# Kernel optimization log

Measured on AMD Instinct MI355X. Metric: run time of the kernel, lower is better.

## Reference

```python
import jax, jax.numpy as jnp
import numpy as np

J = 24          # SMPL_NR_JOINTS
H = 24          # hidden_dim
D_IN = 3        # input_dim (xyz)
SMPL_PARENTS = [-1, 0, 0, 0, 1, 2, 3, 4, 5, 6, 7, 8, 9, 9, 9, 12, 13, 14, 16, 17, 18, 19, 20, 21]

def _build_A():
    # undirected kinematic tree + self loops, row-normalized (mean aggregation)
    M = np.zeros((J, J), np.float32)
    for child, parent in enumerate(SMPL_PARENTS):
        if parent >= 0:
            M[child, parent] = 1.0
            M[parent, child] = 1.0
    M += np.eye(J, dtype=np.float32)
    M /= M.sum(axis=1, keepdims=True)
    return jnp.asarray(M)

A_NORM = _build_A()  # [J, J]

def setup_inputs() -> dict:
    key = jax.random.key(0)
    ks = jax.random.split(key, 12)
    B, S, T = 2048, 24, 24
    g = lambda k, shape, s=0.1: jax.random.normal(k, shape, dtype=jnp.float32) * s
    return {
        "src": g(ks[0], (B, S, J, D_IN), 1.0),
        "tgt": g(ks[1], (B, T, J, D_IN), 1.0),
        "We": g(ks[2], (H, D_IN)), "be": jnp.zeros((H,), jnp.float32),
        # gate order: 0=i, 1=f, 2=c, 3=o
        "Wxl": g(ks[3], (4, H, H)), "bxl": jnp.zeros((4, H), jnp.float32),
        "Wxr": g(ks[4], (4, H, H)),
        "Whl": g(ks[5], (4, H, H)), "bhl": jnp.zeros((4, H), jnp.float32),
        "Whr": g(ks[6], (4, H, H)),
        "wg": g(ks[7], (3, H)),   # peephole weights for i, f, o
        "bg": jnp.zeros((4, H), jnp.float32),
        "Wd": g(ks[8], (D_IN * J, H * J)), "bd": jnp.zeros((D_IN * J,), jnp.float32),
    }

def _gconv(x, Wl, bl, Wr):
    # x: [B, J, D]; mean-aggregate over fixed 24-node graph, then l(agg) + r(x)
    agg = jnp.einsum('ij,bjd->bid', A_NORM, x)
    return agg @ Wl.T + bl + x @ Wr.T

def _cell(X, h, c, Wxl, bxl, Wxr, Whl, bhl, Whr, wg, bg):
    gx = lambda g: _gconv(X, Wxl[g], bxl[g], Wxr[g])
    gh = lambda g: _gconv(h, Whl[g], bhl[g], Whr[g])
    i = jax.nn.sigmoid(gx(0) + gh(0) + wg[0] * c + bg[0])
    f = jax.nn.sigmoid(gx(1) + gh(1) + wg[1] * c + bg[1])
    c_new = f * c + i * jnp.tanh(gx(2) + gh(2) + bg[2])
    o = jax.nn.sigmoid(gx(3) + gh(3) + wg[2] * c_new + bg[3])
    h_new = o * jnp.tanh(c_new)
    return o, h_new, c_new

def reference(src, tgt, We, be, Wxl, bxl, Wxr, Whl, bhl, Whr, wg, bg, Wd, bd):
    B, S = src.shape[0], src.shape[1]
    T = tgt.shape[1]
    params = (Wxl, bxl, Wxr, Whl, bhl, Whr, wg, bg)
    enc = lambda x: jax.nn.relu(x @ We.T + be)  # [B, J, H]

    # --- warm-up over last 24 src frames (deterministic: encode only first step) ---
    X0 = enc(src[:, S - 24])
    h = jnp.zeros((B, J, H), src.dtype)
    c = jnp.zeros((B, J, H), src.dtype)
    out, h, c = _cell(X0, h, c, *params)

    def warm_step(carry, _):
        o_, h_, c_ = carry
        o_, h_, c_ = _cell(o_, h_, c_, *params)
        return (o_, h_, c_), None
    (out, h, c), _ = jax.lax.scan(warm_step, (out, h, c), None, length=23)

    # --- decode T steps: first input is enc(tgt[:,0]), then feed previous out ---
    out0, h, c = _cell(enc(tgt[:, 0]), h, c, *params)

    def dec_step(carry, _):
        o_, h_, c_ = carry
        o2, h2, c2 = _cell(o_, h_, c_, *params)
        return (o2, h2, c2), o2
    _, rest = jax.lax.scan(dec_step, (out0, h, c), None, length=T - 1)  # [T-1, B, J, H]

    seq = jnp.concatenate([out0[None], rest], axis=0)            # [T, B, J, H]
    outs = seq.transpose(1, 0, 2, 3).reshape(B, T, J * H)        # [B, T, 576]
    return outs @ Wd.T + bd                                      # [B, T, 72]
```

## Files before the change

kernel.cpp:

```cpp
#include <hip/hip_runtime.h>


typedef short  s16x8 __attribute__((ext_vector_type(8)));
typedef float  f32x4 __attribute__((ext_vector_type(4)));
typedef _Float16 f16x8 __attribute__((ext_vector_type(8)));

#define TPB 192
#define NB 2
#define PQ_OFF 0
#define UO_OFF 19968
#define SMEM_SZ 26880

#define BAR() do { asm volatile("s_waitcnt lgkmcnt(0)" ::: "memory"); \
                   __builtin_amdgcn_s_barrier(); } while (0)

#define L2E  1.4426950408889634f
#define L2E2 2.8853900817779268f

__device__ __forceinline__ unsigned short f2h(float f) {
    _Float16 h = (_Float16)f;
    return *(unsigned short*)&h;
}
__device__ __forceinline__ unsigned int pkrtz(float a, float b) {
    auto h = __builtin_amdgcn_cvt_pkrtz(a, b);
    return *(unsigned int*)&h;
}
__device__ __forceinline__ float frcp(float x) { return __builtin_amdgcn_rcpf(x); }

#if __has_builtin(__builtin_amdgcn_exp2f)
#define EXP2(x) __builtin_amdgcn_exp2f(x)
#else
#define EXP2(x) __expf((x) * 0.6931471805599453f)
#endif

__device__ __forceinline__ float sigm2(float y) {
    float t = EXP2(-y);
    return frcp(1.0f + t);
}
__device__ __forceinline__ float tanh2s(float ys) {
    float t = EXP2(fminf(-ys, 86.64f));
    return (1.f - t) * frcp(1.f + t);
}
__device__ __forceinline__ float tanhc(float x) {
    float t = EXP2(fminf(x * -L2E2, 86.64f));
    return (1.f - t) * frcp(1.f + t);
}

#if __has_builtin(__builtin_amdgcn_mov_dpp)
__device__ __forceinline__ float xor8(float v) {
    int r = __builtin_amdgcn_mov_dpp(__float_as_int(v), 0x128, 0xf, 0xf, false);
    return __int_as_float(r);
}
#else
__device__ __forceinline__ float xor8(float v) { return __shfl_xor(v, 8); }
#endif

extern "C" __global__ void __launch_bounds__(TPB, 3)
gclstm_main(const float* __restrict__ src,
            const float* __restrict__ tgt,
            const float* __restrict__ We,
            const float* __restrict__ be,
            const float* __restrict__ Wxl,
            const float* __restrict__ bxl,
            const float* __restrict__ Wxr,
            const float* __restrict__ Whl,
            const float* __restrict__ bhl,
            const float* __restrict__ Whr,
            const float* __restrict__ wg,
            const float* __restrict__ bg,
            unsigned short* __restrict__ seqh)
{
    __shared__ __align__(16) char smem[SMEM_SZ];
    unsigned short* PQt  = (unsigned short*)(smem + PQ_OFF);
    unsigned short* UO   = (unsigned short*)(smem + UO_OFF);
    unsigned int*   UO32 = (unsigned int*)(smem + UO_OFF);

    const int tid = threadIdx.x;
    const int b0 = blockIdx.x * NB;
    const int lane = tid & 63, wid = tid >> 6;
    const int l15 = lane & 15, quad = lane >> 4;

    const int par[24] = {-1,0,0,0,1,2,3,4,5,6,7,8,9,9,9,12,13,14,16,17,18,19,20,21};

    f16x8 w1f[4][2];
#pragma unroll
    for (int cj = 0; cj < 4; ++cj) {
        int np = (wid * 4 + cj) * 16 + l15;
        int path = np >= 96 ? 1 : 0;
        int nn = np - path * 96;
        int g = nn / 24, d = nn - g * 24;
        const float* Wx = path ? Wxr : Wxl;
        const float* Wh = path ? Whr : Whl;
#pragma unroll
        for (int kt = 0; kt < 2; ++kt) {
            f16x8 f;
#pragma unroll
            for (int kk = 0; kk < 8; ++kk) {
                int k = kt * 32 + quad * 8 + kk;
                float v = 0.f;
                if (k < 48) {
                    int df = k >> 1;
                    v = (k & 1) ? Wh[g * 576 + d * 24 + df] : Wx[g * 576 + d * 24 + df];
                }
                f[kk] = (_Float16)v;
            }
            w1f[cj][kt] = f;
        }
    }

    f16x8 mf[3];
    {
        int i = wid * 16 + l15;
        int si = i / 24, ji = i - si * 24;
        int cnt = 1 + (par[ji] >= 0 ? 1 : 0);
#pragma unroll
        for (int ch = 0; ch < 24; ++ch) cnt += (par[ch] == ji) ? 1 : 0;
        float cntf = (float)cnt;
#pragma unroll
        for (int kt = 0; kt < 3; ++kt) {
            f16x8 f;
#pragma unroll
            for (int kk = 0; kk < 8; ++kk) {
                int jp = kt * 32 + quad * 8 + kk;
                int sj = jp / 48;
                int rem = jp - sj * 48;
                int pz = rem / 24;
                int j = rem - pz * 24;
                float v = 0.f;
                if (sj == si) {
                    if (pz == 0) v = (j == ji || par[j] == ji || par[ji] == j) ? 1.f : 0.f;
                    else         v = (j == ji) ? cntf : 0.f;
                }
                f[kk] = (_Float16)v;
            }
            mf[kt] = f;
        }
    }

    const int d1 = l15;
    const int d2 = 16 + (l15 & 7);
    const bool lo = l15 < 8;
    float bC1[4], bC2[4], wv1[3], wv2[3];
#pragma unroll
    for (int g = 0; g < 4; ++g) {
        float sc = (g == 2) ? L2E2 : L2E;
        bC1[g] = (bxl[g * 24 + d1] + bhl[g * 24 + d1] + bg[g * 24 + d1]) * sc;
        bC2[g] = (bxl[g * 24 + d2] + bhl[g * 24 + d2] + bg[g * 24 + d2]) * sc;
    }
#pragma unroll
    for (int p = 0; p < 3; ++p) {
        wv1[p] = wg[p * 24 + d1] * L2E;
        wv2[p] = wg[p * 24 + d2] * L2E;
    }

    int rowR[4];
    float iwR1[4], iwR2[4];
    unsigned int sb[4];
#pragma unroll
    for (int rr = 0; rr < 4; ++rr) {
        int row = wid * 16 + quad * 4 + rr;
        rowR[rr] = row;
        int j = row % 24;
        int cnt = 1 + (par[j] >= 0 ? 1 : 0);
#pragma unroll
        for (int ch = 0; ch < 24; ++ch) cnt += (par[ch] == j) ? 1 : 0;
        float iw = cnt == 2 ? 0.5f : cnt == 3 ? (1.f / 3.f) : cnt == 4 ? 0.25f : 0.2f;
        iwR1[rr] = iw * L2E;
        iwR2[rr] = iw * L2E2;
        sb[rr] = (unsigned int)((b0 + row / 24) * 13824 + j * 24);
    }
    int row2v[2]; float iw2v1[2], iw2v2[2]; unsigned int sb2v[2];
#pragma unroll
    for (int e = 0; e < 2; ++e) {
        int rsel = lo ? e : e + 2;
        row2v[e] = rowR[rsel];
        iw2v1[e] = iwR1[rsel]; iw2v2[e] = iwR2[rsel];
        sb2v[e] = sb[rsel];
    }

    float c1[4] = {0.f, 0.f, 0.f, 0.f};
    float c2[2] = {0.f, 0.f};

#pragma unroll
    for (int t = 0; t < 3; ++t) {
        int task = tid + t * TPB;
        int row = task / 12, dp = task - row * 12;
        int b = b0 + row / 24, j = row % 24;
        const float* sp = src + (size_t)b * 1728 + j * 3;
        float s0 = sp[0], s1 = sp[1], s2 = sp[2];
        int d = 2 * dp;
        float x0 = be[d] + s0 * We[d * 3] + s1 * We[d * 3 + 1] + s2 * We[d * 3 + 2];
        float x1 = be[d + 1] + s0 * We[d * 3 + 3] + s1 * We[d * 3 + 4] + s2 * We[d * 3 + 5];
        x0 = fmaxf(x0, 0.f); x1 = fmaxf(x1, 0.f);
        uint2 wv; wv.x = pkrtz(x0, 0.f); wv.y = pkrtz(x1, 0.f);
        *(uint2*)(UO32 + row * 36 + 2 * dp) = wv;
    }
    {
        int row = tid >> 2, c = tid & 3;
        uint2 z; z.x = 0u; z.y = 0u;
        *(uint2*)(UO32 + row * 36 + 24 + 2 * c) = z;
    }
    __syncthreads();

    for (int s = 0; s < 48; ++s) {
        if (s == 24) {
#pragma unroll
            for (int t = 0; t < 3; ++t) {
                int task = tid + t * TPB;
                int row = task / 12, dp = task - row * 12;
                int b = b0 + row / 24, j = row % 24;
                const float* tp = tgt + (size_t)b * 1728 + j * 3;
                float s0 = tp[0], s1 = tp[1], s2 = tp[2];
                int d = 2 * dp;
                float x0 = be[d] + s0 * We[d * 3] + s1 * We[d * 3 + 1] + s2 * We[d * 3 + 2];
                float x1 = be[d + 1] + s0 * We[d * 3 + 3] + s1 * We[d * 3 + 4]
                         + s2 * We[d * 3 + 5];
                x0 = fmaxf(x0, 0.f); x1 = fmaxf(x1, 0.f);
                UO[row * 72 + 4 * dp] = f2h(x0);
                UO[row * 72 + 4 * dp + 2] = f2h(x1);
            }
            BAR();
        }

        f32x4 acc1[3][4];
#pragma unroll
        for (int rt = 0; rt < 3; ++rt)
#pragma unroll
            for (int cj = 0; cj < 4; ++cj) acc1[rt][cj] = (f32x4)0.f;
        __builtin_amdgcn_s_setprio(1);
#pragma unroll
        for (int kt = 0; kt < 2; ++kt) {
            f16x8 a[3];
#pragma unroll
            for (int rt = 0; rt < 3; ++rt)
                a[rt] = *(const f16x8*)(UO + (rt * 16 + l15) * 72 + kt * 32 + quad * 8);
#pragma unroll
            for (int rt = 0; rt < 3; ++rt)
#pragma unroll
                for (int cj = 0; cj < 4; ++cj)
                    acc1[rt][cj] = __builtin_amdgcn_mfma_f32_16x16x32_f16(a[rt], w1f[cj][kt], acc1[rt][cj], 0, 0, 0);
        }
        __builtin_amdgcn_s_setprio(0);
#pragma unroll
        for (int rt = 0; rt < 3; ++rt)
#pragma unroll
            for (int cj = 0; cj < 4; ++cj) {
                int np = (wid * 4 + cj) * 16 + l15;
                int path = np >= 96;
                int nn = np - (path ? 96 : 0);
                int jg = rt * 16 + quad * 4;
                int col = (path ? 24 : 0) + jg + (jg >= 24 ? 24 : 0);
                uint2 wv;
                wv.x = pkrtz(acc1[rt][cj][0], acc1[rt][cj][1]);
                wv.y = pkrtz(acc1[rt][cj][2], acc1[rt][cj][3]);
                *(uint2*)(PQt + nn * 104 + col) = wv;
            }
        BAR();

        f32x4 acc2[6];
#pragma unroll
        for (int nt = 0; nt < 6; ++nt) acc2[nt] = (f32x4)0.f;
        __builtin_amdgcn_s_setprio(1);
#pragma unroll
        for (int kt = 0; kt < 3; ++kt) {
            if (kt == 2 && wid == 0) continue;
            if (kt == 0 && wid == 2) continue;
            f16x8 bf[6];
#pragma unroll
            for (int nt = 0; nt < 6; ++nt)
                bf[nt] = *(const f16x8*)(PQt + (nt * 16 + l15) * 104 + kt * 32 + quad * 8);
#pragma unroll
            for (int nt = 0; nt < 6; ++nt)
                acc2[nt] = __builtin_amdgcn_mfma_f32_16x16x32_f16(mf[kt], bf[nt], acc2[nt], 0, 0, 0);
        }
        __builtin_amdgcn_s_setprio(0);

        const int so = (s - 24) * 576;

#pragma unroll
        for (int rr = 0; rr < 4; ++rr) {
            float pf_s = xor8(lo ? acc2[2][rr] : acc2[1][rr]);
            float po_s = xor8(lo ? acc2[5][rr] : acc2[4][rr]);
            float iw1 = iwR1[rr], iw2 = iwR2[rr];
            int row = rowR[rr];
            float c = c1[rr];
            float pi = fmaf(iw1, acc2[0][rr], bC1[0]);
            float pf = fmaf(iw1, pf_s, bC1[1]);
            float pcs = fmaf(iw2, acc2[3][rr], bC1[2]);
            float po = fmaf(iw1, po_s, bC1[3]);
            float iv = sigm2(fmaf(wv1[0], c, pi));
            float fv = sigm2(fmaf(wv1[1], c, pf));
            float cn = fmaf(fv, c, iv * tanh2s(pcs));
            float ov = sigm2(fmaf(wv1[2], cn, po));
            c1[rr] = cn;
            float hv = ov * tanhc(cn);
            unsigned int pk = pkrtz(ov, hv);
            UO32[row * 36 + d1] = pk;
            if (s >= 24) seqh[sb[rr] + (unsigned int)(so + d1)] = (unsigned short)pk;
        }
#pragma unroll
        for (int e = 0; e < 2; ++e) {
            float sA = xor8(lo ? acc2[1][e + 2] : acc2[2][e]);
            float sB = xor8(lo ? acc2[4][e + 2] : acc2[5][e]);
            float g0 = lo ? acc2[1][e] : sA;
            float g1 = lo ? sA : acc2[2][e + 2];
            float g2 = lo ? acc2[4][e] : sB;
            float g3 = lo ? sB : acc2[5][e + 2];
            float iw1 = iw2v1[e], iw2 = iw2v2[e];
            int row = row2v[e];
            float c = c2[e];
            float pi = fmaf(iw1, g0, bC2[0]);
            float pf = fmaf(iw1, g1, bC2[1]);
            float pcs = fmaf(iw2, g2, bC2[2]);
            float po = fmaf(iw1, g3, bC2[3]);
            float iv = sigm2(fmaf(wv2[0], c, pi));
            float fv = sigm2(fmaf(wv2[1], c, pf));
            float cn = fmaf(fv, c, iv * tanh2s(pcs));
            float ov = sigm2(fmaf(wv2[2], cn, po));
            c2[e] = cn;
            float hv = ov * tanhc(cn);
            unsigned int pk = pkrtz(ov, hv);
            UO32[row * 36 + d2] = pk;
            if (s >= 24) seqh[sb2v[e] + (unsigned int)(so + d2)] = (unsigned short)pk;
        }
        BAR();
    }
}

extern "C" __global__ void __launch_bounds__(256)
wd_conv(const float* __restrict__ Wd, unsigned short* __restrict__ WdH)
{
    int i = blockIdx.x * 256 + threadIdx.x;
    if (i < 46080) {
        int n = i / 576, k = i - n * 576;
        WdH[i] = (n < 72) ? f2h(Wd[n * 576 + k]) : (unsigned short)0;
    }
}

template <int PRECONV>
__global__ void __launch_bounds__(256, 6)
gclstm_proj(const unsigned short* __restrict__ seqh,
            const unsigned short* __restrict__ WdH,
            const float* __restrict__ Wd,
            const float* __restrict__ bd,
            float* __restrict__ out)
{
    __shared__ unsigned short SQ[32 * 104];
    __shared__ unsigned short WH[80 * 104];

    const int tid = threadIdx.x;
    const int R0 = blockIdx.x * 32;
    const int lane = tid & 63, wid = tid >> 6;
    const int l15 = lane & 15, quad = lane >> 4;
    const int rt = wid & 1;
    const int c0 = (wid < 2) ? 0 : 3;
    const int nct = (wid < 2) ? 3 : 2;

    f32x4 acc[3];
#pragma unroll
    for (int j = 0; j < 3; ++j) acc[j] = (f32x4)0.f;

    if (PRECONV) {
        s16x8 sreg[2], wreg[4];
        const int r0s = tid / 12, c0s = tid - r0s * 12;
        const int i1 = tid + 256;
        const int r1s = i1 / 12, c1s = i1 - r1s * 12;
        sreg[0] = *(const s16x8*)(seqh + (size_t)(R0 + r0s) * 576 + (size_t)(c0s * 8));
        if (tid < 128)
            sreg[1] = *(const s16x8*)(seqh + (size_t)(R0 + r1s) * 576 + (size_t)(c1s * 8));
#pragma unroll
        for (int j = 0; j < 4; ++j) {
            int i = tid + j * 256;
            if (i < 960) { int n = i / 12, c8 = i - n * 12;
                wreg[j] = *(const s16x8*)(WdH + (size_t)n * 576 + (size_t)(c8 * 8)); }
        }
        for (int kc = 0; kc < 576; kc += 96) {
            *(s16x8*)(&SQ[r0s * 104 + c0s * 8]) = sreg[0];
            if (tid < 128) *(s16x8*)(&SQ[r1s * 104 + c1s * 8]) = sreg[1];
#pragma unroll
            for (int j = 0; j < 4; ++j) {
                int i = tid + j * 256;
                if (i < 960) { int n = i / 12, c8 = i - n * 12;
                    *(s16x8*)(&WH[n * 104 + c8 * 8]) = wreg[j]; }
            }
            BAR();
            if (kc + 96 < 576) {
                sreg[0] = *(const s16x8*)(seqh + (size_t)(R0 + r0s) * 576 + (size_t)(kc + 96 + c0s * 8));
                if (tid < 128)
                    sreg[1] = *(const s16x8*)(seqh + (size_t)(R0 + r1s) * 576 + (size_t)(kc + 96 + c1s * 8));
#pragma unroll
                for (int j = 0; j < 4; ++j) {
                    int i = tid + j * 256;
                    if (i < 960) { int n = i / 12, c8 = i - n * 12;
                        wreg[j] = *(const s16x8*)(WdH + (size_t)n * 576 + (size_t)(kc + 96 + c8 * 8)); }
                }
            }
#pragma unroll
            for (int kt = 0; kt < 3; ++kt) {
                int koff = kt * 32 + quad * 8;
                f16x8 a = *(const f16x8*)(&SQ[(rt * 16 + l15) * 104 + koff]);
#pragma unroll
                for (int j = 0; j < 3; ++j) {
                    if (j < nct) {
                        f16x8 b = *(const f16x8*)(&WH[((c0 + j) * 16 + l15) * 104 + koff]);
                        acc[j] = __builtin_amdgcn_mfma_f32_16x16x32_f16(a, b, acc[j], 0, 0, 0);
                    }
                }
            }
            BAR();
        }
    } else {
        for (int kc = 0; kc < 576; kc += 96) {
            __syncthreads();
            for (int i = tid; i < 384; i += 256) {
                int r = i / 12, c8 = i - r * 12;
                *(s16x8*)(&SQ[r * 104 + c8 * 8]) =
                    *(const s16x8*)(seqh + (size_t)(R0 + r) * 576 + (size_t)(kc + c8 * 8));
            }
            for (int i = tid; i < 7680; i += 256) {
                int n = i / 96, kk = i - n * 96;
                float v = (n < 72) ? Wd[(size_t)n * 576 + (size_t)(kc + kk)] : 0.f;
                WH[n * 104 + kk] = f2h(v);
            }
            __syncthreads();
#pragma unroll
            for (int kt = 0; kt < 3; ++kt) {
                int koff = kt * 32 + quad * 8;
                f16x8 a = *(const f16x8*)(&SQ[(rt * 16 + l15) * 104 + koff]);
#pragma unroll
                for (int j = 0; j < 3; ++j) {
                    if (j < nct) {
                        f16x8 b = *(const f16x8*)(&WH[((c0 + j) * 16 + l15) * 104 + koff]);
                        acc[j] = __builtin_amdgcn_mfma_f32_16x16x32_f16(a, b, acc[j], 0, 0, 0);
                    }
                }
            }
        }
    }

#pragma unroll
    for (int j = 0; j < 3; ++j) {
        if (j < nct) {
            int n = (c0 + j) * 16 + l15;
            if (n < 72) {
                float bv = bd[n];
                int rbase = R0 + rt * 16 + quad * 4;
#pragma unroll
                for (int r = 0; r < 4; ++r)
                    out[(size_t)(rbase + r) * 72 + (size_t)n] = acc[j][r] + bv;
            }
        }
    }
}

extern "C" void kernel_launch(void* const* d_in, const int* in_sizes, int n_in,
                              void* d_out, int out_size, void* d_ws, size_t ws_size,
                              hipStream_t stream)
{
    const float* src = (const float*)d_in[0];
    const float* tgt = (const float*)d_in[1];
    const float* We  = (const float*)d_in[2];
    const float* be  = (const float*)d_in[3];
    const float* Wxl = (const float*)d_in[4];
    const float* bxl = (const float*)d_in[5];
    const float* Wxr = (const float*)d_in[6];
    const float* Whl = (const float*)d_in[7];
    const float* bhl = (const float*)d_in[8];
    const float* Whr = (const float*)d_in[9];
    const float* wg  = (const float*)d_in[10];
    const float* bg  = (const float*)d_in[11];
    const float* Wd  = (const float*)d_in[12];
    const float* bd  = (const float*)d_in[13];
    float* out = (float*)d_out;
    unsigned short* seqh = (unsigned short*)d_ws;

    const size_t seq_bytes = (size_t)2048 * 24 * 576 * 2;
    unsigned short* WdH = (unsigned short*)((char*)d_ws + seq_bytes);
    const bool preconv = ws_size >= seq_bytes + (size_t)80 * 576 * 2;

    if (preconv)
        wd_conv<<<dim3(180), dim3(256), 0, stream>>>(Wd, WdH);
    gclstm_main<<<dim3(1024), dim3(TPB), 0, stream>>>(
        src, tgt, We, be, Wxl, bxl, Wxr, Whl, bhl, Whr, wg, bg, seqh);
    if (preconv)
        gclstm_proj<1><<<dim3(1536), dim3(256), 0, stream>>>(seqh, WdH, Wd, bd, out);
    else
        gclstm_proj<0><<<dim3(1536), dim3(256), 0, stream>>>(seqh, nullptr, Wd, bd, out);
}
```

Measured before the change: 303.9 us.

## Fuse output projection into recurrent kernel epilogue

```diff
diff --git a/kernel.cpp b/kernel.cpp
--- a/kernel.cpp
+++ b/kernel.cpp
@@ -55,7 +55,8 @@
 __device__ __forceinline__ float xor8(float v) { return __shfl_xor(v, 8); }
 #endif
 
-extern "C" __global__ void __launch_bounds__(TPB, 3)
+template <int FUSE>
+__global__ void __launch_bounds__(TPB, 3)
 gclstm_main(const float* __restrict__ src,
             const float* __restrict__ tgt,
             const float* __restrict__ We,
@@ -68,7 +69,10 @@
             const float* __restrict__ Whr,
             const float* __restrict__ wg,
             const float* __restrict__ bg,
-            unsigned short* __restrict__ seqh)
+            unsigned short* __restrict__ seqh,
+            const unsigned short* __restrict__ WdH,
+            const float* __restrict__ bd,
+            float* __restrict__ out)
 {
     __shared__ __align__(16) char smem[SMEM_SZ];
     unsigned short* PQt  = (unsigned short*)(smem + PQ_OFF);
@@ -325,6 +329,59 @@
         }
         BAR();
     }
+
+    if (FUSE) {
+        asm volatile("s_waitcnt vmcnt(0) lgkmcnt(0)" ::: "memory");
+        __builtin_amdgcn_s_barrier();
+        unsigned short* SQ = (unsigned short*)smem;
+        unsigned short* WH = (unsigned short*)(smem + 9984);
+
+        f32x4 pacc[5];
+#pragma unroll
+        for (int j = 0; j < 5; ++j) pacc[j] = (f32x4)0.f;
+
+        for (int kc = 0; kc < 576; kc += 96) {
+            for (int i = tid; i < 576; i += TPB) {
+                int rl = i / 12, c8 = i - rl * 12;
+                int bl = rl / 24, t = rl - bl * 24;
+                *(s16x8*)(&SQ[rl * 104 + c8 * 8]) =
+                    *(const s16x8*)(seqh + (size_t)(b0 + bl) * 13824
+                                          + (size_t)t * 576 + (size_t)(kc + c8 * 8));
+            }
+            for (int i = tid; i < 960; i += TPB) {
+                int n = i / 12, c8 = i - n * 12;
+                *(s16x8*)(&WH[n * 104 + c8 * 8]) =
+                    *(const s16x8*)(WdH + (size_t)n * 576 + (size_t)(kc + c8 * 8));
+            }
+            BAR();
+            __builtin_amdgcn_s_setprio(1);
+#pragma unroll
+            for (int kt = 0; kt < 3; ++kt) {
+                int koff = kt * 32 + quad * 8;
+                f16x8 a = *(const f16x8*)(&SQ[(wid * 16 + l15) * 104 + koff]);
+#pragma unroll
+                for (int j = 0; j < 5; ++j) {
+                    f16x8 b = *(const f16x8*)(&WH[(j * 16 + l15) * 104 + koff]);
+                    pacc[j] = __builtin_amdgcn_mfma_f32_16x16x32_f16(a, b, pacc[j], 0, 0, 0);
+                }
+            }
+            __builtin_amdgcn_s_setprio(0);
+            BAR();
+        }
+#pragma unroll
+        for (int j = 0; j < 5; ++j) {
+            int n = j * 16 + l15;
+            if (n < 72) {
+                float bv = bd[n];
+#pragma unroll
+                for (int r = 0; r < 4; ++r) {
+                    int rl = wid * 16 + quad * 4 + r;
+                    int bl = rl / 24, t = rl - bl * 24;
+                    out[(size_t)(b0 + bl) * 1728 + (size_t)(t * 72 + n)] = pacc[j][r] + bv;
+                }
+            }
+        }
+    }
 }
 
 extern "C" __global__ void __launch_bounds__(256)
@@ -337,13 +394,11 @@
     }
 }
 
-template <int PRECONV>
 __global__ void __launch_bounds__(256, 6)
-gclstm_proj(const unsigned short* __restrict__ seqh,
-            const unsigned short* __restrict__ WdH,
-            const float* __restrict__ Wd,
-            const float* __restrict__ bd,
-            float* __restrict__ out)
+gclstm_proj_lds(const unsigned short* __restrict__ seqh,
+                const float* __restrict__ Wd,
+                const float* __restrict__ bd,
+                float* __restrict__ out)
 {
     __shared__ unsigned short SQ[32 * 104];
     __shared__ unsigned short WH[80 * 104];
@@ -360,79 +415,28 @@
 #pragma unroll
     for (int j = 0; j < 3; ++j) acc[j] = (f32x4)0.f;
 
-    if (PRECONV) {
-        s16x8 sreg[2], wreg[4];
-        const int r0s = tid / 12, c0s = tid - r0s * 12;
-        const int i1 = tid + 256;
-        const int r1s = i1 / 12, c1s = i1 - r1s * 12;
-        sreg[0] = *(const s16x8*)(seqh + (size_t)(R0 + r0s) * 576 + (size_t)(c0s * 8));
-        if (tid < 128)
-            sreg[1] = *(const s16x8*)(seqh + (size_t)(R0 + r1s) * 576 + (size_t)(c1s * 8));
-#pragma unroll
-        for (int j = 0; j < 4; ++j) {
-            int i = tid + j * 256;
-            if (i < 960) { int n = i / 12, c8 = i - n * 12;
-                wreg[j] = *(const s16x8*)(WdH + (size_t)n * 576 + (size_t)(c8 * 8)); }
-        }
-        for (int kc = 0; kc < 576; kc += 96) {
-            *(s16x8*)(&SQ[r0s * 104 + c0s * 8]) = sreg[0];
-            if (tid < 128) *(s16x8*)(&SQ[r1s * 104 + c1s * 8]) = sreg[1];
-#pragma unroll
-            for (int j = 0; j < 4; ++j) {
-                int i = tid + j * 256;
-                if (i < 960) { int n = i / 12, c8 = i - n * 12;
-                    *(s16x8*)(&WH[n * 104 + c8 * 8]) = wreg[j]; }
-            }
-            BAR();
-            if (kc + 96 < 576) {
-                sreg[0] = *(const s16x8*)(seqh + (size_t)(R0 + r0s) * 576 + (size_t)(kc + 96 + c0s * 8));
-                if (tid < 128)
-                    sreg[1] = *(const s16x8*)(seqh + (size_t)(R0 + r1s) * 576 + (size_t)(kc + 96 + c1s * 8));
-#pragma unroll
-                for (int j = 0; j < 4; ++j) {
-                    int i = tid + j * 256;
-                    if (i < 960) { int n = i / 12, c8 = i - n * 12;
-                        wreg[j] = *(const s16x8*)(WdH + (size_t)n * 576 + (size_t)(kc + 96 + c8 * 8)); }
-                }
-            }
-#pragma unroll
-            for (int kt = 0; kt < 3; ++kt) {
-                int koff = kt * 32 + quad * 8;
-                f16x8 a = *(const f16x8*)(&SQ[(rt * 16 + l15) * 104 + koff]);
-#pragma unroll
-                for (int j = 0; j < 3; ++j) {
-                    if (j < nct) {
-                        f16x8 b = *(const f16x8*)(&WH[((c0 + j) * 16 + l15) * 104 + koff]);
-                        acc[j] = __builtin_amdgcn_mfma_f32_16x16x32_f16(a, b, acc[j], 0, 0, 0);
-                    }
-                }
-            }
-            BAR();
-        }
-    } else {
-        for (int kc = 0; kc < 576; kc += 96) {
-            __syncthreads();
-            for (int i = tid; i < 384; i += 256) {
-                int r = i / 12, c8 = i - r * 12;
-                *(s16x8*)(&SQ[r * 104 + c8 * 8]) =
-                    *(const s16x8*)(seqh + (size_t)(R0 + r) * 576 + (size_t)(kc + c8 * 8));
-            }
-            for (int i = tid; i < 7680; i += 256) {
-                int n = i / 96, kk = i - n * 96;
-                float v = (n < 72) ? Wd[(size_t)n * 576 + (size_t)(kc + kk)] : 0.f;
-                WH[n * 104 + kk] = f2h(v);
-            }
-            __syncthreads();
-#pragma unroll
-            for (int kt = 0; kt < 3; ++kt) {
-                int koff = kt * 32 + quad * 8;
-                f16x8 a = *(const f16x8*)(&SQ[(rt * 16 + l15) * 104 + koff]);
-#pragma unroll
-                for (int j = 0; j < 3; ++j) {
-                    if (j < nct) {
-                        f16x8 b = *(const f16x8*)(&WH[((c0 + j) * 16 + l15) * 104 + koff]);
-                        acc[j] = __builtin_amdgcn_mfma_f32_16x16x32_f16(a, b, acc[j], 0, 0, 0);
-                    }
+    for (int kc = 0; kc < 576; kc += 96) {
+        __syncthreads();
+        for (int i = tid; i < 384; i += 256) {
+            int r = i / 12, c8 = i - r * 12;
+            *(s16x8*)(&SQ[r * 104 + c8 * 8]) =
+                *(const s16x8*)(seqh + (size_t)(R0 + r) * 576 + (size_t)(kc + c8 * 8));
+        }
+        for (int i = tid; i < 7680; i += 256) {
+            int n = i / 96, kk = i - n * 96;
+            float v = (n < 72) ? Wd[(size_t)n * 576 + (size_t)(kc + kk)] : 0.f;
+            WH[n * 104 + kk] = f2h(v);
+        }
+        __syncthreads();
+#pragma unroll
+        for (int kt = 0; kt < 3; ++kt) {
+            int koff = kt * 32 + quad * 8;
+            f16x8 a = *(const f16x8*)(&SQ[(rt * 16 + l15) * 104 + koff]);
+#pragma unroll
+            for (int j = 0; j < 3; ++j) {
+                if (j < nct) {
+                    f16x8 b = *(const f16x8*)(&WH[((c0 + j) * 16 + l15) * 104 + koff]);
+                    acc[j] = __builtin_amdgcn_mfma_f32_16x16x32_f16(a, b, acc[j], 0, 0, 0);
                 }
             }
         }
@@ -478,12 +482,15 @@
     unsigned short* WdH = (unsigned short*)((char*)d_ws + seq_bytes);
     const bool preconv = ws_size >= seq_bytes + (size_t)80 * 576 * 2;
 
-    if (preconv)
+    if (preconv) {
         wd_conv<<<dim3(180), dim3(256), 0, stream>>>(Wd, WdH);
-    gclstm_main<<<dim3(1024), dim3(TPB), 0, stream>>>(
-        src, tgt, We, be, Wxl, bxl, Wxr, Whl, bhl, Whr, wg, bg, seqh);
-    if (preconv)
-        gclstm_proj<1><<<dim3(1536), dim3(256), 0, stream>>>(seqh, WdH, Wd, bd, out);
-    else
-        gclstm_proj<0><<<dim3(1536), dim3(256), 0, stream>>>(seqh, nullptr, Wd, bd, out);
-}
+        gclstm_main<1><<<dim3(1024), dim3(TPB), 0, stream>>>(
+            src, tgt, We, be, Wxl, bxl, Wxr, Whl, bhl, Whr, wg, bg,
+            seqh, WdH, bd, out);
+    } else {
+        gclstm_main<0><<<dim3(1024), dim3(TPB), 0, stream>>>(
+            src, tgt, We, be, Wxl, bxl, Wxr, Whl, bhl, Whr, wg, bg,
+            seqh, nullptr, bd, out);
+        gclstm_proj_lds<<<dim3(1536), dim3(256), 0, stream>>>(seqh, Wd, bd, out);
+    }
+}
```

Measured after the change: 319.0 us. +5.0%, slower.

## Permute PQt column layout so wave 1 skips one K-tile of aggregation MFMA

Applied to the files above, without the earlier changes.

```diff
diff --git a/kernel.cpp b/kernel.cpp
--- a/kernel.cpp
+++ b/kernel.cpp
@@ -81,6 +81,13 @@
     const int l15 = lane & 15, quad = lane >> 4;
 
     const int par[24] = {-1,0,0,0,1,2,3,4,5,6,7,8,9,9,9,12,13,14,16,17,18,19,20,21};
+    const int QP[2][2][6] = {
+        { {8,9,10,11,12,13}, {0,1,2,3,14,15} },
+        { {4,5,6,16,17,18},  {7,19,20,21,22,23} }
+    };
+    const int IS[24] = {0,0,0,0, 1,1,1,1, 0,0,0,0,0,0,0,0, 1,1,1,1,1,1,1,1};
+    const int IP[24] = {1,1,1,1, 0,0,0,1, 0,0,0,0,0,0,1,1, 0,0,0,1,1,1,1,1};
+    const int IQ[24] = {0,1,2,3, 0,1,2,0, 0,1,2,3,4,5,4,5, 3,4,5,1,2,3,4,5};
 
     f16x8 w1f[4][2];
 #pragma unroll
@@ -108,13 +115,26 @@
         }
     }
 
+    int colT[3][4];
+#pragma unroll
+    for (int rt = 0; rt < 3; ++rt)
+#pragma unroll
+        for (int cj = 0; cj < 4; ++cj) {
+            int np = (wid * 4 + cj) * 16 + l15;
+            int path = np >= 96 ? 1 : 0;
+            int jg = rt * 16 + quad * 4;
+            int sm = jg >= 24 ? 1 : 0;
+            int jm = jg - sm * 24;
+            colT[rt][cj] = QP[sm][path][jm >> 2] * 4;
+        }
+
     f16x8 mf[3];
     {
-        int i = wid * 16 + l15;
-        int si = i / 24, ji = i - si * 24;
-        int cnt = 1 + (par[ji] >= 0 ? 1 : 0);
-#pragma unroll
-        for (int ch = 0; ch < 24; ++ch) cnt += (par[ch] == ji) ? 1 : 0;
+        int rs = (wid == 0) ? 0 : (wid == 1) ? 1 : (l15 < 8 ? 0 : 1);
+        int rj = (wid < 2) ? l15 : 16 + (l15 & 7);
+        int cnt = 1 + (par[rj] >= 0 ? 1 : 0);
+#pragma unroll
+        for (int ch = 0; ch < 24; ++ch) cnt += (par[ch] == rj) ? 1 : 0;
         float cntf = (float)cnt;
 #pragma unroll
         for (int kt = 0; kt < 3; ++kt) {
@@ -122,14 +142,14 @@
 #pragma unroll
             for (int kk = 0; kk < 8; ++kk) {
                 int jp = kt * 32 + quad * 8 + kk;
-                int sj = jp / 48;
-                int rem = jp - sj * 48;
-                int pz = rem / 24;
-                int j = rem - pz * 24;
+                int slot = jp >> 2, pos = jp & 3;
+                int j = IQ[slot] * 4 + pos;
                 float v = 0.f;
-                if (sj == si) {
-                    if (pz == 0) v = (j == ji || par[j] == ji || par[ji] == j) ? 1.f : 0.f;
-                    else         v = (j == ji) ? cntf : 0.f;
+                if (IS[slot] == rs) {
+                    if (IP[slot] == 0)
+                        v = (j == rj || par[j] == rj || par[rj] == j) ? 1.f : 0.f;
+                    else
+                        v = (j == rj) ? cntf : 0.f;
                 }
                 f[kk] = (_Float16)v;
             }
@@ -158,16 +178,17 @@
     unsigned int sb[4];
 #pragma unroll
     for (int rr = 0; rr < 4; ++rr) {
-        int row = wid * 16 + quad * 4 + rr;
-        rowR[rr] = row;
-        int j = row % 24;
+        int li = quad * 4 + rr;
+        int sm = (wid == 0) ? 0 : (wid == 1) ? 1 : (li < 8 ? 0 : 1);
+        int j = (wid < 2) ? li : 16 + (li & 7);
+        rowR[rr] = sm * 24 + j;
         int cnt = 1 + (par[j] >= 0 ? 1 : 0);
 #pragma unroll
         for (int ch = 0; ch < 24; ++ch) cnt += (par[ch] == j) ? 1 : 0;
         float iw = cnt == 2 ? 0.5f : cnt == 3 ? (1.f / 3.f) : cnt == 4 ? 0.25f : 0.2f;
         iwR1[rr] = iw * L2E;
         iwR2[rr] = iw * L2E2;
-        sb[rr] = (unsigned int)((b0 + row / 24) * 13824 + j * 24);
+        sb[rr] = (unsigned int)((b0 + sm) * 13824 + j * 24);
     }
     int row2v[2]; float iw2v1[2], iw2v2[2]; unsigned int sb2v[2];
 #pragma unroll
@@ -246,14 +267,11 @@
 #pragma unroll
             for (int cj = 0; cj < 4; ++cj) {
                 int np = (wid * 4 + cj) * 16 + l15;
-                int path = np >= 96;
-                int nn = np - (path ? 96 : 0);
-                int jg = rt * 16 + quad * 4;
-                int col = (path ? 24 : 0) + jg + (jg >= 24 ? 24 : 0);
+                int nn = np - (np >= 96 ? 96 : 0);
                 uint2 wv;
                 wv.x = pkrtz(acc1[rt][cj][0], acc1[rt][cj][1]);
                 wv.y = pkrtz(acc1[rt][cj][2], acc1[rt][cj][3]);
-                *(uint2*)(PQt + nn * 104 + col) = wv;
+                *(uint2*)(PQt + nn * 104 + colT[rt][cj]) = wv;
             }
         BAR();
 
@@ -264,6 +282,7 @@
 #pragma unroll
         for (int kt = 0; kt < 3; ++kt) {
             if (kt == 2 && wid == 0) continue;
+            if (kt == 1 && wid == 1) continue;
             if (kt == 0 && wid == 2) continue;
             f16x8 bf[6];
 #pragma unroll
```

New measurement: 304.8 us. No clear change (+0.3%).
